# Performance work log

Hardware: AMD Instinct MI355X
Metric: run time of the kernel (lower is better)

The kernel has to match this reference:

```python
import jax, jax.numpy as jnp
import numpy as np

N = 10000       # nodes
E = 200000      # node pairs (edges) in rel_dict
R = 400000      # relation instances
F_IN = 128
F_OUT = 64


def setup_inputs() -> dict:
    key = jax.random.key(0)
    ks = jax.random.split(key, 8)
    x = jax.random.normal(ks[0], (N, F_IN), dtype=jnp.float32)
    rel = jax.random.normal(ks[1], (R, F_IN), dtype=jnp.float32)
    adj = jax.random.uniform(ks[2], (N, N), dtype=jnp.float32)
    edge_pairs = jax.random.randint(ks[3], (E, 2), 0, N, dtype=jnp.int32)
    rel_seg = jax.random.randint(ks[4], (R,), 0, E, dtype=jnp.int32)
    # Conv1d(in, out, kernel_size=1, bias=False) == Linear: weight [out, in]
    W = jax.random.normal(ks[5], (F_OUT, F_IN), dtype=jnp.float32) * 0.1
    w_rel = jax.random.normal(ks[6], (F_IN,), dtype=jnp.float32) * 0.1
    bias = jnp.zeros((F_OUT,), dtype=jnp.float32)
    return {"x": x, "rel": rel, "adj": adj, "edge_pairs": edge_pairs,
            "rel_seg": rel_seg, "W": W, "w_rel": w_rel, "bias": bias}


def reference(x, rel, adj, edge_pairs, rel_seg, W, w_rel, bias):
    # node transform: [N, F_OUT]
    seq_fts = x @ W.T
    # per-relation scalar: [R]
    fts_rel = rel @ w_rel
    # segment-mean per edge (vectorized form of the rel_dict loop)
    sums = jax.ops.segment_sum(fts_rel, rel_seg, num_segments=E)
    cnts = jax.ops.segment_sum(jnp.ones_like(fts_rel), rel_seg, num_segments=E)
    edge_means = sums / jnp.maximum(cnts, 1.0)  # [E]
    # symmetric scatter into dense logits [N, N]
    e1, e2 = edge_pairs[:, 0], edge_pairs[:, 1]
    logits = jnp.zeros_like(adj)
    logits = logits.at[e1, e2].set(edge_means).at[e2, e1].set(edge_means)
    # masked-ish softmax over rows, then sparse-weighted aggregation
    coefs = jax.nn.softmax(jax.nn.sigmoid(logits) + adj, axis=1)  # [N, N]
    # dropout is a no-op in eval mode (training=False)
    ret = coefs @ seq_fts + bias  # [N, F_OUT]
    return jax.nn.elu(ret)        # concat=True
```

## Files before the change

### kernel.cpp

```cpp
#include <hip/hip_runtime.h>
#include <math.h>

#define NN   10000
#define EE   200000
#define RR   400000
#define FIN  128
#define FOUT 64
#define NK   10048

#define HASH_BITS 20
#define HSIZE (1u << HASH_BITS)
#define HMASK (HSIZE - 1u)
#define ROWCAP 256

typedef __bf16 bf16x8 __attribute__((ext_vector_type(8)));
typedef float  f32x4  __attribute__((ext_vector_type(4)));

#define O_SUMS   0
#define O_CNTS   (O_SUMS + EE)
#define O_ROWCNT (O_CNTS + EE)
#define O_HKEY   (O_ROWCNT + NN)
#define O_HPRIO  (O_HKEY + HSIZE)
#define O_SEQT   (O_HPRIO + HSIZE)
#define ZERO_WORDS (O_SEQT + (FOUT * NK) / 2)
#define O_SEQ    ZERO_WORDS
#define O_NUMP   (O_SEQ + NN * FOUT)
#define O_SP     (O_NUMP + 8 * NN * FOUT)
#define O_PAIRS  (O_SP + 8 * NN)

__global__ __launch_bounds__(256) void k_zero(f32x4* __restrict__ p, int n4) {
    int gid = blockIdx.x * 256 + threadIdx.x;
    if (gid < n4) p[gid] = (f32x4){0.f, 0.f, 0.f, 0.f};
}

__global__ __launch_bounds__(256) void k_seqfts(const float* __restrict__ x,
                                                const float* __restrict__ W,
                                                float* __restrict__ seq,
                                                __bf16* __restrict__ seqT) {
    __shared__ float Wt[FIN][FOUT + 1];
    __shared__ float xs[FIN][16 + 1];
    int t = threadIdx.x;
    for (int e = t; e < FOUT * FIN; e += 256) {
        int c = e >> 7, k = e & 127;
        Wt[k][c] = W[e];
    }
    int row0 = blockIdx.x * 16;
    for (int e = t; e < 16 * FIN; e += 256) {
        int r = e >> 7, k = e & 127;
        int gr = row0 + r;
        xs[k][r] = (gr < NN) ? x[(size_t)gr * FIN + k] : 0.f;
    }
    __syncthreads();
    int col = t & 63;
    int rg  = t >> 6;
    float acc[4] = {0.f, 0.f, 0.f, 0.f};
    for (int k = 0; k < FIN; ++k) {
        float w = Wt[k][col];
        #pragma unroll
        for (int i = 0; i < 4; ++i) acc[i] += w * xs[k][rg * 4 + i];
    }
    #pragma unroll
    for (int i = 0; i < 4; ++i) {
        int gr = row0 + rg * 4 + i;
        if (gr < NN) {
            seq[(size_t)gr * FOUT + col] = acc[i];
            seqT[(size_t)col * NK + gr] = (__bf16)acc[i];
        }
    }
}

__device__ __forceinline__ unsigned hash_cell(unsigned cell) {
    return (cell * 2654435761u) >> (32 - HASH_BITS);
}
__device__ __forceinline__ void entry_ij(const int* ep, int e, int& i, int& j, int& k) {
    k = (e < EE) ? e : e - EE;
    int a = ep[2 * k], b = ep[2 * k + 1];
    if (e < EE) { i = a; j = b; } else { i = b; j = a; }
}

#define BK 64
#define KSPLIT 8
#define NCHUNK 157
#define CPK 20
#define NSTRIP (NN / 16)
#define MAINW (NSTRIP * KSPLIT)
#define RELW  (RR / 16)
#define HASHW ((2 * EE + 63) / 64)
#define TOTW  (MAINW + RELW + HASHW)
#define GRID_MR ((TOTW + 3) / 4)

__global__ __launch_bounds__(256, 4) void k_mainrel(const float* __restrict__ adj,
                                                    const __bf16* __restrict__ seqT,
                                                    const float* __restrict__ rel,
                                                    const float* __restrict__ wrel,
                                                    const int* __restrict__ rseg,
                                                    const int* __restrict__ ep,
                                                    float* __restrict__ sums,
                                                    float* __restrict__ cnts,
                                                    unsigned* __restrict__ hkey,
                                                    unsigned* __restrict__ hprio,
                                                    float* __restrict__ Nump,
                                                    float* __restrict__ Sp) {
    int t   = threadIdx.x;
    int wid = blockIdx.x * 4 + (t >> 6);
    int l   = t & 63;

    if (wid < MAINW) {
        int strip = wid % NSTRIP;
        int ks    = wid / NSTRIP;
        int row0  = strip * 16;
        int c0 = ks * CPK, c1 = min(NCHUNK, c0 + CPK);
        int lr = l & 15, lk = l >> 4;
        const float*  arow  = adj  + (size_t)(row0 + lr) * NN;
        const __bf16* bbase = seqT + (size_t)lr * NK;

        f32x4 acc[4];
        #pragma unroll
        for (int n = 0; n < 4; ++n) acc[n] = (f32x4){0.f, 0.f, 0.f, 0.f};
        float rs = 0.f;

        for (int ch = c0; ch < c1; ++ch) {
            int k0 = ch * BK;
            #pragma unroll
            for (int h = 0; h < 2; ++h) {
                int gk = k0 + h * 32 + lk * 8;
                f32x4 a0 = (f32x4){-1e9f, -1e9f, -1e9f, -1e9f};
                f32x4 a1 = a0;
                if (gk < NN) {
                    a0 = *(const f32x4*)(arow + gk);
                    a1 = *(const f32x4*)(arow + gk + 4);
                }
                float w0 = __expf(a0.x + 0.5f);
                float w1 = __expf(a0.y + 0.5f);
                float w2 = __expf(a0.z + 0.5f);
                float w3 = __expf(a0.w + 0.5f);
                float w4 = __expf(a1.x + 0.5f);
                float w5 = __expf(a1.y + 0.5f);
                float w6 = __expf(a1.z + 0.5f);
                float w7 = __expf(a1.w + 0.5f);
                rs += ((w0 + w1) + (w2 + w3)) + ((w4 + w5) + (w6 + w7));
                bf16x8 af = { (__bf16)w0, (__bf16)w1, (__bf16)w2, (__bf16)w3,
                              (__bf16)w4, (__bf16)w5, (__bf16)w6, (__bf16)w7 };
                const __bf16* bp = bbase + gk;
                #pragma unroll
                for (int n = 0; n < 4; ++n) {
                    bf16x8 b = *(const bf16x8*)(bp + (size_t)n * 16 * NK);
                    acc[n] = __builtin_amdgcn_mfma_f32_16x16x32_bf16(af, b, acc[n], 0, 0, 0);
                }
            }
        }
        rs += __shfl_xor(rs, 16, 64);
        rs += __shfl_xor(rs, 32, 64);
        if (lk == 0) Sp[(size_t)ks * NN + row0 + lr] = rs;
        float* nout = Nump + (size_t)ks * NN * FOUT;
        #pragma unroll
        for (int n = 0; n < 4; ++n) {
            #pragma unroll
            for (int r = 0; r < 4; ++r)
                nout[(size_t)(row0 + lk * 4 + r) * FOUT + n * 16 + lr] = acc[n][r];
        }
        return;
    }

    if (wid < MAINW + RELW) {
        int rw   = wid - MAINW;
        int lane = l & 31;
        int half = l >> 5;
        f32x4 wv = *(const f32x4*)(wrel + lane * 4);
        #pragma unroll
        for (int it = 0; it < 8; ++it) {
            int row = rw * 16 + it * 2 + half;
            f32x4 v = *(const f32x4*)(rel + (size_t)row * FIN + lane * 4);
            float s = v.x * wv.x + v.y * wv.y + v.z * wv.z + v.w * wv.w;
            #pragma unroll
            for (int off = 16; off >= 1; off >>= 1) s += __shfl_xor(s, off, 64);
            if (lane == 0) {
                int seg = rseg[row];
                atomicAdd(&sums[seg], s);
                atomicAdd(&cnts[seg], 1.0f);
            }
        }
        return;
    }

    {
        int e = (wid - MAINW - RELW) * 64 + l;
        if (e >= 2 * EE) return;
        int i, j, k;
        entry_ij(ep, e, i, j, k);
        unsigned cell = (unsigned)i * NN + (unsigned)j;
        unsigned keyv = cell + 1u;
        unsigned h = hash_cell(cell);
        while (true) {
            unsigned old = atomicCAS(&hkey[h], 0u, keyv);
            if (old == 0u || old == keyv) break;
            h = (h + 1u) & HMASK;
        }
        atomicMax(&hprio[h], (unsigned)(e + 1));
    }
}

__global__ __launch_bounds__(256) void k_scatB(const int* __restrict__ ep,
                                               const float* __restrict__ sums,
                                               const float* __restrict__ cnts,
                                               const unsigned* __restrict__ hkey,
                                               const unsigned* __restrict__ hprio,
                                               const float* __restrict__ adj,
                                               int* __restrict__ rowcnt,
                                               uint2* __restrict__ pairs) {
    int e = blockIdx.x * 256 + threadIdx.x;
    if (e >= 2 * EE) return;
    int i, j, k;
    entry_ij(ep, e, i, j, k);
    unsigned cell = (unsigned)i * NN + (unsigned)j;
    unsigned keyv = cell + 1u;
    unsigned h = hash_cell(cell);
    while (hkey[h] != keyv) h = (h + 1u) & HMASK;
    if (hprio[h] == (unsigned)(e + 1)) {
        float v   = sums[k] / fmaxf(cnts[k], 1.0f);
        float sg  = 1.f / (1.f + __expf(-v));
        float aij = adj[(size_t)i * NN + j];
        float dw  = __expf(aij + sg) - __expf(aij + 0.5f);
        if (dw != 0.f) {
            int pos = atomicAdd(&rowcnt[i], 1);
            if (pos < ROWCAP)
                pairs[(size_t)i * ROWCAP + pos] =
                    make_uint2((unsigned)j, __float_as_uint(dw));
        }
    }
}

__global__ __launch_bounds__(256) void k_rowupd(const float* __restrict__ Nump,
                                                const float* __restrict__ Sp,
                                                const int* __restrict__ rowcnt,
                                                const uint2* __restrict__ pairs,
                                                const float* __restrict__ seq,
                                                const float* __restrict__ bias,
                                                float* __restrict__ out) {
    int t = threadIdx.x;
    int i = blockIdx.x * 4 + (t >> 6);
    if (i >= NN) return;
    int c = t & 63;
    float acc = 0.f, sb = 0.f;
    #pragma unroll
    for (int ks = 0; ks < 8; ++ks) {
        acc += Nump[(size_t)ks * NN * FOUT + (size_t)i * FOUT + c];
        sb  += Sp[(size_t)ks * NN + i];
    }
    int cnt = min(rowcnt[i], ROWCAP);
    float sdw = 0.f;
    const uint2* pr = pairs + (size_t)i * ROWCAP;
    #pragma unroll 4
    for (int e = 0; e < cnt; ++e) {
        uint2 pk = pr[e];
        float d  = __uint_as_float(pk.y);
        acc += d * seq[(size_t)pk.x * FOUT + c];
        sdw += d;
    }
    float v = acc / (sb + sdw) + bias[c];
    out[(size_t)i * FOUT + c] = (v > 0.f) ? v : expm1f(v);
}

extern "C" void kernel_launch(void* const* d_in, const int* in_sizes, int n_in,
                              void* d_out, int out_size, void* d_ws, size_t ws_size,
                              hipStream_t stream) {
    const float* x    = (const float*)d_in[0];
    const float* rel  = (const float*)d_in[1];
    const float* adj  = (const float*)d_in[2];
    const int*   ep   = (const int*)d_in[3];
    const int*   rseg = (const int*)d_in[4];
    const float* W    = (const float*)d_in[5];
    const float* wrel = (const float*)d_in[6];
    const float* bias = (const float*)d_in[7];
    float* out = (float*)d_out;

    float* ws = (float*)d_ws;
    float*    sums   = ws + O_SUMS;
    float*    cnts   = ws + O_CNTS;
    int*      rowcnt = (int*)(ws + O_ROWCNT);
    unsigned* hkey   = (unsigned*)(ws + O_HKEY);
    unsigned* hprio  = (unsigned*)(ws + O_HPRIO);
    __bf16*   seqT   = (__bf16*)(ws + O_SEQT);
    float*    seq    = ws + O_SEQ;
    float*    Nump   = ws + O_NUMP;
    float*    Sp     = ws + O_SP;
    uint2*    pairs  = (uint2*)(ws + O_PAIRS);

    int n4 = ZERO_WORDS / 4;
    k_zero<<<(n4 + 255) / 256, 256, 0, stream>>>((f32x4*)d_ws, n4);
    k_seqfts<<<NN / 16, 256, 0, stream>>>(x, W, seq, seqT);
    k_mainrel<<<GRID_MR, 256, 0, stream>>>(adj, seqT, rel, wrel, rseg, ep,
                                           sums, cnts, hkey, hprio, Nump, Sp);
    k_scatB<<<(2 * EE + 255) / 256, 256, 0, stream>>>(ep, sums, cnts, hkey, hprio,
                                                      adj, rowcnt, pairs);
    k_rowupd<<<(NN + 3) / 4, 256, 0, stream>>>(Nump, Sp, rowcnt, pairs,
                                               seq, bias, out);
}
```

Baseline: 310.4 us.

## Pre-pack seq features in MFMA layout, stage adj tiles via LDS, fold rowsum into MFMA

Stores the bf16 transposed node features in a pre-swizzled block layout matching the MFMA B-operand, so each lane loads one contiguous 16-byte fragment per K-block. It adds a fifth column block of ones so the softmax denominator comes out of the matrix multiply instead of a separate shuffle reduction. Adjacency rows are read coalesced (each lane covers 4 consecutive columns across 16 rows), software-prefetched one chunk ahead, exponentiated with exp2, and staged through LDS before forming A fragments. The strip/k-split mapping of waves is interleaved, and the fp32 seq copy is dropped, with the sparse row update reading bf16 from the packed layout. This costs extra MFMA work for the ones block, more register pressure from the 16-vector prefetch, and some precision in the sparse correction.

```diff
diff --git a/kernel.cpp b/kernel.cpp
--- a/kernel.cpp
+++ b/kernel.cpp
@@ -6,14 +6,17 @@
 #define RR   400000
 #define FIN  128
 #define FOUT 64
-#define NK   10048
 
 #define HASH_BITS 20
 #define HSIZE (1u << HASH_BITS)
 #define HMASK (HSIZE - 1u)
 #define ROWCAP 256
 
+#define NKB 314
+#define LDB 264
+
 typedef __bf16 bf16x8 __attribute__((ext_vector_type(8)));
+typedef __bf16 bf16x4 __attribute__((ext_vector_type(4)));
 typedef float  f32x4  __attribute__((ext_vector_type(4)));
 
 #define O_SUMS   0
@@ -21,10 +24,10 @@
 #define O_ROWCNT (O_CNTS + EE)
 #define O_HKEY   (O_ROWCNT + NN)
 #define O_HPRIO  (O_HKEY + HSIZE)
-#define O_SEQT   (O_HPRIO + HSIZE)
-#define ZERO_WORDS (O_SEQT + (FOUT * NK) / 2)
-#define O_SEQ    ZERO_WORDS
-#define O_NUMP   (O_SEQ + NN * FOUT)
+#define O_SEQTP  (O_HPRIO + HSIZE)
+#define SEQTP_WORDS (NKB * 5 * 512 / 2)
+#define ZERO_WORDS (O_SEQTP + SEQTP_WORDS)
+#define O_NUMP   ZERO_WORDS
 #define O_SP     (O_NUMP + 8 * NN * FOUT)
 #define O_PAIRS  (O_SP + 8 * NN)
 
@@ -35,8 +38,7 @@
 
 __global__ __launch_bounds__(256) void k_seqfts(const float* __restrict__ x,
                                                 const float* __restrict__ W,
-                                                float* __restrict__ seq,
-                                                __bf16* __restrict__ seqT) {
+                                                __bf16* __restrict__ seqTp) {
     __shared__ float Wt[FIN][FOUT + 1];
     __shared__ float xs[FIN][16 + 1];
     int t = threadIdx.x;
@@ -62,10 +64,11 @@
     #pragma unroll
     for (int i = 0; i < 4; ++i) {
         int gr = row0 + rg * 4 + i;
-        if (gr < NN) {
-            seq[(size_t)gr * FOUT + col] = acc[i];
-            seqT[(size_t)col * NK + gr] = (__bf16)acc[i];
-        }
+        int kb = gr >> 5, g = (gr >> 3) & 3, slot = gr & 7;
+        seqTp[((size_t)kb * 5 + (col >> 4)) * 512 + ((col & 15) + g * 16) * 8 + slot]
+            = (__bf16)acc[i];
+        if (col < 16)
+            seqTp[((size_t)kb * 5 + 4) * 512 + (col + g * 16) * 8 + slot] = (__bf16)1.0f;
     }
 }
 
@@ -78,11 +81,10 @@
     if (e < EE) { i = a; j = b; } else { i = b; j = a; }
 }
 
-#define BK 64
 #define KSPLIT 8
-#define NCHUNK 157
-#define CPK 20
 #define NSTRIP (NN / 16)
+#define CPW 5
+#define CHK 256
 #define MAINW (NSTRIP * KSPLIT)
 #define RELW  (RR / 16)
 #define HASHW ((2 * EE + 63) / 64)
@@ -90,7 +92,7 @@
 #define GRID_MR ((TOTW + 3) / 4)
 
 __global__ __launch_bounds__(256, 4) void k_mainrel(const float* __restrict__ adj,
-                                                    const __bf16* __restrict__ seqT,
+                                                    const __bf16* __restrict__ seqTp,
                                                     const float* __restrict__ rel,
                                                     const float* __restrict__ wrel,
                                                     const int* __restrict__ rseg,
@@ -101,63 +103,82 @@
                                                     unsigned* __restrict__ hprio,
                                                     float* __restrict__ Nump,
                                                     float* __restrict__ Sp) {
+    __shared__ __bf16 atile[4][16 * LDB];
     int t   = threadIdx.x;
     int wid = blockIdx.x * 4 + (t >> 6);
     int l   = t & 63;
 
     if (wid < MAINW) {
-        int strip = wid % NSTRIP;
-        int ks    = wid / NSTRIP;
+        int strip = wid >> 3;
+        int ks    = wid & 7;
         int row0  = strip * 16;
-        int c0 = ks * CPK, c1 = min(NCHUNK, c0 + CPK);
         int lr = l & 15, lk = l >> 4;
-        const float*  arow  = adj  + (size_t)(row0 + lr) * NN;
-        const __bf16* bbase = seqT + (size_t)lr * NK;
-
-        f32x4 acc[4];
-        #pragma unroll
-        for (int n = 0; n < 4; ++n) acc[n] = (f32x4){0.f, 0.f, 0.f, 0.f};
-        float rs = 0.f;
-
-        for (int ch = c0; ch < c1; ++ch) {
-            int k0 = ch * BK;
-            #pragma unroll
-            for (int h = 0; h < 2; ++h) {
-                int gk = k0 + h * 32 + lk * 8;
-                f32x4 a0 = (f32x4){-1e9f, -1e9f, -1e9f, -1e9f};
-                f32x4 a1 = a0;
-                if (gk < NN) {
-                    a0 = *(const f32x4*)(arow + gk);
-                    a1 = *(const f32x4*)(arow + gk + 4);
+        __bf16* my = &atile[t >> 6][0];
+
+        f32x4 acc[5];
+        #pragma unroll
+        for (int n = 0; n < 5; ++n) acc[n] = (f32x4){0.f, 0.f, 0.f, 0.f};
+
+        f32x4 pv[16];
+        int c0 = ks * CPW;
+
+        {
+            int k0 = c0 * CHK;
+            bool ok = (k0 + 4 * l) < NN;
+            #pragma unroll
+            for (int r = 0; r < 16; ++r) {
+                f32x4 v = (f32x4){-1e9f, -1e9f, -1e9f, -1e9f};
+                if (ok) v = *(const f32x4*)(adj + (size_t)(row0 + r) * NN + k0 + 4 * l);
+                pv[r] = v;
+            }
+        }
+
+        #pragma unroll
+        for (int c = 0; c < CPW; ++c) {
+            int k0 = (c0 + c) * CHK;
+            #pragma unroll
+            for (int r = 0; r < 16; ++r) {
+                float e0 = exp2f(fmaf(pv[r].x, 1.442695041f, 0.7213475204f));
+                float e1 = exp2f(fmaf(pv[r].y, 1.442695041f, 0.7213475204f));
+                float e2 = exp2f(fmaf(pv[r].z, 1.442695041f, 0.7213475204f));
+                float e3 = exp2f(fmaf(pv[r].w, 1.442695041f, 0.7213475204f));
+                bf16x4 q = { (__bf16)e0, (__bf16)e1, (__bf16)e2, (__bf16)e3 };
+                *(bf16x4*)&my[r * LDB + l * 4] = q;
+            }
+            if (c + 1 < CPW) {
+                int kn = (c0 + c + 1) * CHK;
+                bool ok = (kn + 4 * l) < NN;
+                #pragma unroll
+                for (int r = 0; r < 16; ++r) {
+                    f32x4 v = (f32x4){-1e9f, -1e9f, -1e9f, -1e9f};
+                    if (ok) v = *(const f32x4*)(adj + (size_t)(row0 + r) * NN + kn + 4 * l);
+                    pv[r] = v;
                 }
-                float w0 = __expf(a0.x + 0.5f);
-                float w1 = __expf(a0.y + 0.5f);
-                float w2 = __expf(a0.z + 0.5f);
-                float w3 = __expf(a0.w + 0.5f);
-                float w4 = __expf(a1.x + 0.5f);
-                float w5 = __expf(a1.y + 0.5f);
-                float w6 = __expf(a1.z + 0.5f);
-                float w7 = __expf(a1.w + 0.5f);
-                rs += ((w0 + w1) + (w2 + w3)) + ((w4 + w5) + (w6 + w7));
-                bf16x8 af = { (__bf16)w0, (__bf16)w1, (__bf16)w2, (__bf16)w3,
-                              (__bf16)w4, (__bf16)w5, (__bf16)w6, (__bf16)w7 };
-                const __bf16* bp = bbase + gk;
+            }
+            int kb0  = k0 >> 5;
+            int hmax = min(8, (NN - k0 + 31) >> 5);
+            for (int h = 0; h < hmax; ++h) {
+                bf16x8 af = *(const bf16x8*)&my[lr * LDB + lk * 8 + h * 32];
+                const __bf16* bp = seqTp + (size_t)(kb0 + h) * 5 * 512 + l * 8;
                 #pragma unroll
-                for (int n = 0; n < 4; ++n) {
-                    bf16x8 b = *(const bf16x8*)(bp + (size_t)n * 16 * NK);
+                for (int n = 0; n < 5; ++n) {
+                    bf16x8 b = *(const bf16x8*)(bp + n * 512);
                     acc[n] = __builtin_amdgcn_mfma_f32_16x16x32_bf16(af, b, acc[n], 0, 0, 0);
                 }
             }
         }
-        rs += __shfl_xor(rs, 16, 64);
-        rs += __shfl_xor(rs, 32, 64);
-        if (lk == 0) Sp[(size_t)ks * NN + row0 + lr] = rs;
+
         float* nout = Nump + (size_t)ks * NN * FOUT;
         #pragma unroll
         for (int n = 0; n < 4; ++n) {
             #pragma unroll
             for (int r = 0; r < 4; ++r)
                 nout[(size_t)(row0 + lk * 4 + r) * FOUT + n * 16 + lr] = acc[n][r];
+        }
+        if (lr == 0) {
+            #pragma unroll
+            for (int r = 0; r < 4; ++r)
+                Sp[(size_t)ks * NN + row0 + lk * 4 + r] = acc[4][r];
         }
         return;
     }
@@ -234,7 +255,7 @@
                                                 const float* __restrict__ Sp,
                                                 const int* __restrict__ rowcnt,
                                                 const uint2* __restrict__ pairs,
-                                                const float* __restrict__ seq,
+                                                const __bf16* __restrict__ seqTp,
                                                 const float* __restrict__ bias,
                                                 float* __restrict__ out) {
     int t = threadIdx.x;
@@ -250,11 +271,13 @@
     int cnt = min(rowcnt[i], ROWCAP);
     float sdw = 0.f;
     const uint2* pr = pairs + (size_t)i * ROWCAP;
-    #pragma unroll 4
     for (int e = 0; e < cnt; ++e) {
         uint2 pk = pr[e];
         float d  = __uint_as_float(pk.y);
-        acc += d * seq[(size_t)pk.x * FOUT + c];
+        unsigned j = pk.x;
+        float sj = (float)seqTp[((size_t)(j >> 5) * 5 + (c >> 4)) * 512
+                                + ((c & 15) + ((j >> 3) & 3) * 16) * 8 + (j & 7)];
+        acc += d * sj;
         sdw += d;
     }
     float v = acc / (sb + sdw) + bias[c];
@@ -280,19 +303,18 @@
     int*      rowcnt = (int*)(ws + O_ROWCNT);
     unsigned* hkey   = (unsigned*)(ws + O_HKEY);
     unsigned* hprio  = (unsigned*)(ws + O_HPRIO);
-    __bf16*   seqT   = (__bf16*)(ws + O_SEQT);
-    float*    seq    = ws + O_SEQ;
+    __bf16*   seqTp  = (__bf16*)(ws + O_SEQTP);
     float*    Nump   = ws + O_NUMP;
     float*    Sp     = ws + O_SP;
     uint2*    pairs  = (uint2*)(ws + O_PAIRS);
 
     int n4 = ZERO_WORDS / 4;
     k_zero<<<(n4 + 255) / 256, 256, 0, stream>>>((f32x4*)d_ws, n4);
-    k_seqfts<<<NN / 16, 256, 0, stream>>>(x, W, seq, seqT);
-    k_mainrel<<<GRID_MR, 256, 0, stream>>>(adj, seqT, rel, wrel, rseg, ep,
+    k_seqfts<<<NN / 16, 256, 0, stream>>>(x, W, seqTp);
+    k_mainrel<<<GRID_MR, 256, 0, stream>>>(adj, seqTp, rel, wrel, rseg, ep,
                                            sums, cnts, hkey, hprio, Nump, Sp);
     k_scatB<<<(2 * EE + 255) / 256, 256, 0, stream>>>(ep, sums, cnts, hkey, hprio,
                                                       adj, rowcnt, pairs);
     k_rowupd<<<(NN + 3) / 4, 256, 0, stream>>>(Nump, Sp, rowcnt, pairs,
-                                               seq, bias, out);
-}
+                                               seqTp, bias, out);
+}
```

Result: slower. 320.0 us (+3.1%).
